# Performance work log

Hardware: AMD Instinct MI355X
Metric: run time of the kernel (lower is better)

## Reference

```python
import jax, jax.numpy as jnp
import numpy as np

TEMP = 0.02          # init kwarg temp (sim is multiplied by temp before exp)
OTHERWEIGHT = 0.5    # init kwarg otherweight (cross-half weighting)


def _labels(overlap_inds, bs):
    # labels1: class i for group i of feats1; labels2: same class if overlap,
    # else a fresh class starting at K, incrementing per non-overlap group.
    K = overlap_inds.shape[0]
    labels1 = jnp.repeat(jnp.arange(K), bs)
    non = (overlap_inds == 0).astype(jnp.int32)
    excl = jnp.cumsum(non) - non  # exclusive prefix count of non-overlap groups
    cls2 = jnp.where(overlap_inds.astype(bool), jnp.arange(K), K + excl)
    labels2 = jnp.repeat(cls2, bs)
    return jnp.concatenate([labels1, labels2])


def setup_inputs() -> dict:
    key = jax.random.key(0)
    k1, k2, k3 = jax.random.split(key, 3)
    K, BS, F = 8, 256, 512
    feats1 = jax.random.normal(k1, (K * BS, F), dtype=jnp.float32)
    feats2 = jax.random.normal(k2, (K * BS, F), dtype=jnp.float32)
    overlap_inds = jax.random.randint(k3, (K,), 0, 2).astype(jnp.int32)
    return {"feats1": feats1, "feats2": feats2, "overlap_inds": overlap_inds, "bs": BS}


def reference(feats1, feats2, overlap_inds, bs):
    n1 = feats1.shape[0]
    feats = jnp.concatenate([feats1, feats2])         # [N, F]
    n = feats.shape[0]
    labels = _labels(overlap_inds, bs)                # [N]

    same = labels[None, :] == labels[:, None]         # [N, N] bool
    sim = jnp.exp((feats @ feats.T) * TEMP)           # [N, N]

    eye = jnp.eye(n, dtype=bool)
    pos_mask = same & ~eye
    neg_mask = ~same

    # cross_weighting: OTHERWEIGHT on cross-half blocks, 1.0 within each half
    half = jnp.arange(n) < n1
    cross = jnp.where(half[:, None] == half[None, :], 1.0, OTHERWEIGHT)

    # per-row negative sum; loss = sum over positives of cw * -log(pos/neg_sum)
    neg_sum = jnp.sum(jnp.where(neg_mask, sim, 0.0), axis=1)        # [N]
    loss_terms = jnp.where(pos_mask, cross * -jnp.log(sim / neg_sum[:, None]), 0.0)
    total_pos = jnp.sum(pos_mask).astype(jnp.float32)
    loss = loss_terms.sum() / total_pos

    # accuracy: a positive counts iff it beats every negative in its row
    # (mean(0)==1.0 over strict > comparisons <=> pos > max(neg))
    max_neg = jnp.max(jnp.where(neg_mask, sim, -jnp.inf), axis=1)   # [N]
    correct = jnp.where(pos_mask, (sim > max_neg[:, None]).astype(jnp.float32), 0.0)
    acc = correct.sum() / total_pos
    return acc, loss
```

## Files before the change

kernel.cpp:

```cpp
#include <hip/hip_runtime.h>


#define KGRP 8
#define FD   512
#define N1T  2048
#define NT   4096
#define TEMPW 0.02f

typedef __attribute__((ext_vector_type(8))) short short8;
typedef __attribute__((ext_vector_type(4))) float f32x4;
typedef unsigned short ushort_t;


__device__ __forceinline__ unsigned enc_ord(float f) {
  unsigned u = __float_as_uint(f);
  return (u & 0x80000000u) ? ~u : (u | 0x80000000u);
}
__device__ __forceinline__ float dec_ord(unsigned u) {
  unsigned b = (u & 0x80000000u) ? (u & 0x7fffffffu) : ~u;
  return __uint_as_float(b);
}

__device__ __forceinline__ ushort_t f2bf(float f) {
  unsigned u = __float_as_uint(f);
  u = (u + 0x7fffu + ((u >> 16) & 1u)) >> 16;
  return (ushort_t)u;
}

__device__ __forceinline__ void gld16(const void* g, void* l) {
  __builtin_amdgcn_global_load_lds(
      (const __attribute__((address_space(1))) unsigned*)g,
      (__attribute__((address_space(3))) unsigned*)l, 16, 0, 0);
}

__global__ __launch_bounds__(256) void prep_k(
    const float* __restrict__ f1, const float* __restrict__ f2,
    ushort_t* __restrict__ bf,
    float* __restrict__ neg_sum, unsigned* __restrict__ neg_max,
    float* __restrict__ sumS, float* __restrict__ corr,
    int* __restrict__ cnts, int* __restrict__ neg_list,
    int* __restrict__ pos_list, const int* __restrict__ ov)
{
  const int b = blockIdx.x, t = threadIdx.x;

  {
    int i = b * 256 + t;
    size_t base = (size_t)i * 8;
    const size_t half = (size_t)N1T * FD;
    const float* sp = (base < half) ? (f1 + base) : (f2 + (base - half));
    float4 u0 = ((const float4*)sp)[0];
    float4 u1 = ((const float4*)sp)[1];
    short8 o;
    o[0] = (short)f2bf(u0.x); o[1] = (short)f2bf(u0.y);
    o[2] = (short)f2bf(u0.z); o[3] = (short)f2bf(u0.w);
    o[4] = (short)f2bf(u1.x); o[5] = (short)f2bf(u1.y);
    o[6] = (short)f2bf(u1.z); o[7] = (short)f2bf(u1.w);
    *(short8*)(bf + base) = o;
  }

  if (b >= 1 && b <= 16) {
    int i = (b - 1) * 256 + t;
    neg_sum[i] = 0.f;
    neg_max[i] = 0u;
  }

  if (b == 0) {
    __shared__ int c[16];
    if (t == 0) {
      sumS[0] = 0.f; corr[0] = 0.f;
      cnts[0] = 0; cnts[1] = 0; cnts[2] = 0;
      int excl = 0;
      for (int g = 0; g < KGRP; g++) c[g] = g;
      for (int g = 0; g < KGRP; g++) {
        if (ov[g]) c[KGRP + g] = g;
        else       { c[KGRP + g] = KGRP + excl; excl++; }
      }
    }
    __syncthreads();
    for (int p = t; p < 1024; p += 256) {
      int bi = p >> 5, bj = p & 31;
      if (bj < bi) continue;
      if (c[bi >> 1] == c[bj >> 1]) {
        int k = atomicAdd(&cnts[1], 1); pos_list[k] = (bi << 5) | bj;
      } else {
        int k = atomicAdd(&cnts[0], 1); neg_list[k] = (bi << 5) | bj;
      }
    }
  }
}

__global__ __launch_bounds__(256, 2) void gram_k(
    const ushort_t* __restrict__ bf, const int* __restrict__ cnts,
    const int* __restrict__ neg_list, const int* __restrict__ pos_list,
    float* __restrict__ neg_sum, unsigned* __restrict__ neg_max,
    float* __restrict__ pos_dots)
{
  __shared__ char lds[4 * 16384];

  const int nn = cnts[0];
  const int b  = blockIdx.x;
  const bool isneg = (b < nn);
  const int pr = isneg ? neg_list[b] : pos_list[b - nn];
  const int bi = pr >> 5, bj = pr & 31;
  const int brow = bi << 7, bcol = bj << 7;

  const int t    = threadIdx.x;
  const int lane = t & 63, wave = t >> 6;
  const int wrow = (wave >> 1) << 6, wcol = (wave & 1) << 6;
  const int fr   = lane & 15, fh = lane >> 4;

  const int r_in = t >> 2;
  const int csw  = (((t & 3) ^ ((t >> 3) & 3)) << 3);
  const ushort_t* gA = bf + (size_t)(brow + r_in) * FD + csw;
  const ushort_t* gB = bf + (size_t)(bcol + r_in) * FD + csw;
  const int ldsw = wave << 10;

  const int fx = ((fh ^ ((fr >> 1) & 3)) << 4);
  int offA[4], offB[4];
#pragma unroll
  for (int m = 0; m < 4; m++) offA[m] = ((wrow + (m << 4) + fr) << 6) + fx;
#pragma unroll
  for (int n = 0; n < 4; n++) offB[n] = 8192 + ((wcol + (n << 4) + fr) << 6) + fx;

  f32x4 acc[4][4];
#pragma unroll
  for (int m = 0; m < 4; m++)
#pragma unroll
    for (int n = 0; n < 4; n++)
      acc[m][n] = (f32x4){0.f, 0.f, 0.f, 0.f};

  auto stage = [&](int s) {
    char* dst = lds + ((s & 3) * 16384) + ldsw;
    const ushort_t* a = gA + (s << 5);
    const ushort_t* p = gB + (s << 5);
    gld16(a,                   dst);
    gld16(a + (size_t)64 * FD, dst + 4096);
    gld16(p,                   dst + 8192);
    gld16(p + (size_t)64 * FD, dst + 12288);
  };

  stage(0); stage(1); stage(2);

#pragma unroll
  for (int s = 0; s < 16; s++) {
    if (s < 14)       asm volatile("s_waitcnt vmcnt(8)" ::: "memory");
    else if (s == 14) asm volatile("s_waitcnt vmcnt(4)" ::: "memory");
    else              asm volatile("s_waitcnt vmcnt(0)" ::: "memory");
    __builtin_amdgcn_s_barrier();
    asm volatile("" ::: "memory");

    char* base = lds + (s & 3) * 16384;
    short8 a[4], bb[4];
#pragma unroll
    for (int m = 0; m < 4; m++) a[m]  = *(const short8*)(base + offA[m]);
#pragma unroll
    for (int n = 0; n < 4; n++) bb[n] = *(const short8*)(base + offB[n]);

    if (s + 3 < 16) stage(s + 3);

#pragma unroll
    for (int m = 0; m < 4; m++)
#pragma unroll
      for (int n = 0; n < 4; n++)
        acc[m][n] = __builtin_amdgcn_mfma_f32_16x16x32_bf16(a[m], bb[n], acc[m][n], 0, 0, 0);
  }

  const int rbase = brow + wrow + (fh << 2);
  const int cbase = bcol + wcol + fr;

  if (isneg) {
    float colS[4] = {0.f, 0.f, 0.f, 0.f};
    float colM[4] = {-3.0e38f, -3.0e38f, -3.0e38f, -3.0e38f};
#pragma unroll
    for (int m = 0; m < 4; m++) {
#pragma unroll
      for (int j = 0; j < 4; j++) {
        float s = 0.f, mx = -3.0e38f;
#pragma unroll
        for (int n = 0; n < 4; n++) {
          float d = acc[m][n][j];
          float e = __expf(d * TEMPW);
          s += e; mx = fmaxf(mx, d);
          colS[n] += e; colM[n] = fmaxf(colM[n], d);
        }
#pragma unroll
        for (int o = 1; o < 16; o <<= 1) {
          s  += __shfl_xor(s, o, 64);
          mx  = fmaxf(mx, __shfl_xor(mx, o, 64));
        }
        if (fr == 0) {
          int r = rbase + (m << 4) + j;
          atomicAdd(&neg_sum[r], s);
          atomicMax(&neg_max[r], enc_ord(mx));
        }
      }
    }
#pragma unroll
    for (int n = 0; n < 4; n++) {
      float s = colS[n], mx = colM[n];
      s += __shfl_xor(s, 16, 64); mx = fmaxf(mx, __shfl_xor(mx, 16, 64));
      s += __shfl_xor(s, 32, 64); mx = fmaxf(mx, __shfl_xor(mx, 32, 64));
      if (fh == 0) {
        int c = cbase + (n << 4);
        atomicAdd(&neg_sum[c], s);
        atomicMax(&neg_max[c], enc_ord(mx));
      }
    }
  } else {
    float* basep = pos_dots + (size_t)(b - nn) * 16384;
#pragma unroll
    for (int m = 0; m < 4; m++)
#pragma unroll
      for (int n = 0; n < 4; n++)
        *(f32x4*)(basep + (((m << 2) + n) << 10) + (t << 2)) = acc[m][n];
  }
}

__global__ __launch_bounds__(256) void pos_fin_k(
    const float* __restrict__ pos_dots, const int* __restrict__ cnts,
    const int* __restrict__ pos_list, const unsigned* __restrict__ neg_max,
    const float* __restrict__ neg_sum, const int* __restrict__ ov,
    float* __restrict__ sumS, float* __restrict__ corr,
    int* __restrict__ done, float* __restrict__ out)
{
  const int np = cnts[1];
  const int p  = blockIdx.x;
  const int t  = threadIdx.x, lane = t & 63, wave = t >> 6;

  __shared__ float wsum[4];
  __shared__ int   wcnt[4];
  __shared__ int   amLast;

  if (p < np) {
    const int pr = pos_list[p];
    const int bi = pr >> 5, bj = pr & 31;
    const int wrow = (wave >> 1) << 6, wcol = (wave & 1) << 6;
    const int fr = lane & 15, fh = lane >> 4;
    const int rbase = (bi << 7) + wrow + (fh << 2);
    const int cbase = (bj << 7) + wcol + fr;
    const float cw = ((bi < 16) == (bj < 16)) ? 1.0f : 0.5f;
    const float* basep = pos_dots + (size_t)p * 16384;

    float ssum = 0.f;
    int cc = 0;
    if (bi == bj) {
#pragma unroll
      for (int m = 0; m < 4; m++)
#pragma unroll
        for (int n = 0; n < 4; n++) {
          f32x4 v = *(const f32x4*)(basep + (((m << 2) + n) << 10) + (t << 2));
          int c = cbase + (n << 4);
#pragma unroll
          for (int j = 0; j < 4; j++) {
            int r = rbase + (m << 4) + j;
            if (r != c) {
              float d = v[j];
              ssum += d;
              cc += (d > dec_ord(neg_max[r])) ? 1 : 0;
            }
          }
        }
    } else {
      float nmr[4][4], nmc[4];
#pragma unroll
      for (int m = 0; m < 4; m++)
#pragma unroll
        for (int j = 0; j < 4; j++) nmr[m][j] = dec_ord(neg_max[rbase + (m << 4) + j]);
#pragma unroll
      for (int n = 0; n < 4; n++) nmc[n] = dec_ord(neg_max[cbase + (n << 4)]);
#pragma unroll
      for (int m = 0; m < 4; m++)
#pragma unroll
        for (int n = 0; n < 4; n++) {
          f32x4 v = *(const f32x4*)(basep + (((m << 2) + n) << 10) + (t << 2));
#pragma unroll
          for (int j = 0; j < 4; j++) {
            float d = v[j];
            ssum += d;
            cc += ((d > nmr[m][j]) ? 1 : 0) + ((d > nmc[n]) ? 1 : 0);
          }
        }
      ssum *= 2.0f;
    }
    ssum *= cw;

#pragma unroll
    for (int o = 1; o < 64; o <<= 1) {
      ssum += __shfl_xor(ssum, o, 64);
      cc   += __shfl_xor(cc, o, 64);
    }
    if (lane == 0) { wsum[wave] = ssum; wcnt[wave] = cc; }
    __syncthreads();
    if (t == 0) {
      float S2 = 0.f; int C2 = 0;
      for (int w = 0; w < 4; w++) { S2 += wsum[w]; C2 += wcnt[w]; }
      atomicAdd(sumS, S2);
      atomicAdd(corr, (float)C2);
    }
  }

  if (t == 0) {
    int my = -1;
    if (p < np) { __threadfence(); my = atomicAdd(done, 1); }
    amLast = (my == np - 1) ? 1 : 0;
  }
  __syncthreads();
  if (!amLast) return;
  __threadfence();

  float aa = 0.f;
  for (int r = t; r < NT; r += 256) {
    int g = r >> 8;
    float W = ov[g & 7] ? 383.f : 255.f;
    aa += W * __logf(neg_sum[r]);
  }
#pragma unroll
  for (int o = 1; o < 64; o <<= 1) aa += __shfl_xor(aa, o, 64);
  if (lane == 0) wsum[wave] = aa;
  __syncthreads();
  if (t == 0) {
    float sw = wsum[0] + wsum[1] + wsum[2] + wsum[3];
    float S = atomicAdd(sumS, 0.f);
    float C = atomicAdd(corr, 0.f);
    float tp = 0.f;
    for (int g = 0; g < 16; g++) tp += 256.f * (255.f + 256.f * (ov[g & 7] ? 1.f : 0.f));
    out[0] = C / tp;
    out[1] = (sw - TEMPW * S) / tp;
  }
}


extern "C" void kernel_launch(void* const* d_in, const int* in_sizes, int n_in,
                              void* d_out, int out_size, void* d_ws, size_t ws_size,
                              hipStream_t stream)
{
  const float* f1 = (const float*)d_in[0];
  const float* f2 = (const float*)d_in[1];
  const int*   ov = (const int*)d_in[2];

  char* ws = (char*)d_ws;
  ushort_t* bf       = (ushort_t*)ws;
  float*    neg_sum  = (float*)(ws + (size_t)(4 << 20));
  unsigned* neg_max  = (unsigned*)(ws + (size_t)(4 << 20) + (16 << 10));
  float*    sumS     = (float*)(ws + (size_t)(4 << 20) + (32 << 10));
  float*    corr     = sumS + 1;
  int*      cnts     = (int*)(sumS + 2);
  int*      done     = cnts + 2;
  int*      neg_list = (int*)(ws + (size_t)(4 << 20) + (36 << 10));
  int*      pos_list = (int*)(ws + (size_t)(4 << 20) + (40 << 10));
  float*    pos_dots = (float*)(ws + (size_t)(4 << 20) + (64 << 10));
  float*    out      = (float*)d_out;

  hipLaunchKernelGGL(prep_k, dim3(1024), dim3(256), 0, stream,
                     f1, f2, bf, neg_sum, neg_max, sumS, corr, cnts,
                     neg_list, pos_list, ov);
  hipLaunchKernelGGL(gram_k, dim3(528), dim3(256), 0, stream,
                     bf, cnts, neg_list, pos_list, neg_sum, neg_max, pos_dots);
  hipLaunchKernelGGL(pos_fin_k, dim3(80), dim3(256), 0, stream,
                     pos_dots, cnts, pos_list, neg_max, neg_sum, ov,
                     sumS, corr, done, out);
}
```

Baseline: 49.16 us.

## Give each wave a private LDS slice to drop block barriers in GEMM loop

Each wave now loads only the A rows and B columns it consumes into its own double-buffered LDS region, so the per-k-step block-wide s_barrier is removed and only vmcnt waits remain. This trades shared reuse across waves for independence. Global traffic per block doubles, because each A and B row slice is fetched by two waves instead of one. Pipeline depth also drops from three stages ahead to one.

```diff
diff --git a/kernel.cpp b/kernel.cpp
--- a/kernel.cpp
+++ b/kernel.cpp
@@ -109,18 +109,19 @@
   const int wrow = (wave >> 1) << 6, wcol = (wave & 1) << 6;
   const int fr   = lane & 15, fh = lane >> 4;
 
-  const int r_in = t >> 2;
-  const int csw  = (((t & 3) ^ ((t >> 3) & 3)) << 3);
-  const ushort_t* gA = bf + (size_t)(brow + r_in) * FD + csw;
-  const ushort_t* gB = bf + (size_t)(bcol + r_in) * FD + csw;
-  const int ldsw = wave << 10;
+  char* myLds = lds + wave * 16384;
+
+  const int rq  = lane >> 2;
+  const int csw = ((lane & 3) ^ ((lane >> 3) & 3)) << 3;
+  const ushort_t* gA = bf + (size_t)(brow + wrow + rq) * FD + csw;
+  const ushort_t* gB = bf + (size_t)(bcol + wcol + rq) * FD + csw;
 
   const int fx = ((fh ^ ((fr >> 1) & 3)) << 4);
   int offA[4], offB[4];
 #pragma unroll
-  for (int m = 0; m < 4; m++) offA[m] = ((wrow + (m << 4) + fr) << 6) + fx;
-#pragma unroll
-  for (int n = 0; n < 4; n++) offB[n] = 8192 + ((wcol + (n << 4) + fr) << 6) + fx;
+  for (int m = 0; m < 4; m++) offA[m] = (((m << 4) + fr) << 6) + fx;
+#pragma unroll
+  for (int n = 0; n < 4; n++) offB[n] = 4096 + (((n << 4) + fr) << 6) + fx;
 
   f32x4 acc[4][4];
 #pragma unroll
@@ -129,34 +130,34 @@
     for (int n = 0; n < 4; n++)
       acc[m][n] = (f32x4){0.f, 0.f, 0.f, 0.f};
 
-  auto stage = [&](int s) {
-    char* dst = lds + ((s & 3) * 16384) + ldsw;
+  auto stageW = [&](int s) {
+    char* dst = myLds + ((s & 1) << 13);
     const ushort_t* a = gA + (s << 5);
     const ushort_t* p = gB + (s << 5);
-    gld16(a,                   dst);
-    gld16(a + (size_t)64 * FD, dst + 4096);
-    gld16(p,                   dst + 8192);
-    gld16(p + (size_t)64 * FD, dst + 12288);
+    gld16(a,         dst);
+    gld16(a +  8192, dst + 1024);
+    gld16(a + 16384, dst + 2048);
+    gld16(a + 24576, dst + 3072);
+    gld16(p,         dst + 4096);
+    gld16(p +  8192, dst + 5120);
+    gld16(p + 16384, dst + 6144);
+    gld16(p + 24576, dst + 7168);
   };
 
-  stage(0); stage(1); stage(2);
+  stageW(0);
 
 #pragma unroll
   for (int s = 0; s < 16; s++) {
-    if (s < 14)       asm volatile("s_waitcnt vmcnt(8)" ::: "memory");
-    else if (s == 14) asm volatile("s_waitcnt vmcnt(4)" ::: "memory");
-    else              asm volatile("s_waitcnt vmcnt(0)" ::: "memory");
-    __builtin_amdgcn_s_barrier();
-    asm volatile("" ::: "memory");
-
-    char* base = lds + (s & 3) * 16384;
+    if (s + 1 < 16) stageW(s + 1);
+    if (s + 1 < 16) asm volatile("s_waitcnt vmcnt(8)" ::: "memory");
+    else            asm volatile("s_waitcnt vmcnt(0)" ::: "memory");
+
+    char* base = myLds + ((s & 1) << 13);
     short8 a[4], bb[4];
 #pragma unroll
     for (int m = 0; m < 4; m++) a[m]  = *(const short8*)(base + offA[m]);
 #pragma unroll
     for (int n = 0; n < 4; n++) bb[n] = *(const short8*)(base + offB[n]);
-
-    if (s + 3 < 16) stage(s + 3);
 
 #pragma unroll
     for (int m = 0; m < 4; m++)
```

Measured after the change: 54.08 us. 1.1x slower.

## Fuse gram and positive-finalize kernels via atomic job queue and spin-wait

Applied to the files above, without the earlier changes.

Merges the gram and positive-finalization kernels into one persistent-style kernel. Each block takes a job index from an atomic ticket, so negative tiles are handed out first. Positive-tile blocks spin until every negative tile has published its row max, then finish their accuracy and loss terms straight from registers. This removes the pos_dots round-trip through global memory and one kernel launch. In exchange, positive blocks can idle while they wait, and the scheme depends on ticket ordering to avoid deadlock.

```diff
diff --git a/kernel.cpp b/kernel.cpp
--- a/kernel.cpp
+++ b/kernel.cpp
@@ -32,6 +32,7 @@
       (const __attribute__((address_space(1))) unsigned*)g,
       (__attribute__((address_space(3))) unsigned*)l, 16, 0, 0);
 }
+
 
 __global__ __launch_bounds__(256) void prep_k(
     const float* __restrict__ f1, const float* __restrict__ f2,
@@ -68,7 +69,7 @@
     __shared__ int c[16];
     if (t == 0) {
       sumS[0] = 0.f; corr[0] = 0.f;
-      cnts[0] = 0; cnts[1] = 0; cnts[2] = 0;
+      cnts[0] = 0; cnts[1] = 0; cnts[2] = 0; cnts[3] = 0; cnts[4] = 0;
       int excl = 0;
       for (int g = 0; g < KGRP; g++) c[g] = g;
       for (int g = 0; g < KGRP; g++) {
@@ -89,22 +90,27 @@
   }
 }
 
-__global__ __launch_bounds__(256, 2) void gram_k(
-    const ushort_t* __restrict__ bf, const int* __restrict__ cnts,
+__global__ __launch_bounds__(256, 2) void main_k(
+    const ushort_t* __restrict__ bf, int* __restrict__ cnts,
     const int* __restrict__ neg_list, const int* __restrict__ pos_list,
     float* __restrict__ neg_sum, unsigned* __restrict__ neg_max,
-    float* __restrict__ pos_dots)
+    float* __restrict__ sumS, float* __restrict__ corr,
+    const int* __restrict__ ov, float* __restrict__ out)
 {
   __shared__ char lds[4 * 16384];
-
-  const int nn = cnts[0];
-  const int b  = blockIdx.x;
-  const bool isneg = (b < nn);
-  const int pr = isneg ? neg_list[b] : pos_list[b - nn];
+  __shared__ int jid_sh;
+  __shared__ int amLast;
+
+  const int t = threadIdx.x;
+  if (t == 0) jid_sh = atomicAdd(&cnts[2], 1);
+  __syncthreads();
+  const int k  = jid_sh;
+  const int nn = cnts[0], np = cnts[1];
+  const bool isneg = (k < nn);
+  const int pr = isneg ? neg_list[k] : pos_list[k - nn];
   const int bi = pr >> 5, bj = pr & 31;
   const int brow = bi << 7, bcol = bj << 7;
 
-  const int t    = threadIdx.x;
   const int lane = t & 63, wave = t >> 6;
   const int wrow = (wave >> 1) << 6, wcol = (wave & 1) << 6;
   const int fr   = lane & 15, fh = lane >> 4;
@@ -206,113 +212,89 @@
         atomicMax(&neg_max[c], enc_ord(mx));
       }
     }
+    __syncthreads();
+    if (t == 0) { __threadfence(); atomicAdd(&cnts[3], 1); }
+    return;
+  }
+
+  if (t == 0) {
+    while (atomicAdd(&cnts[3], 0) < nn) __builtin_amdgcn_s_sleep(8);
+  }
+  __syncthreads();
+
+  float* nmf = (float*)lds;
+  if (t < 128) nmf[t] = dec_ord(atomicAdd(&neg_max[brow + t], 0u));
+  else         nmf[t] = dec_ord(atomicAdd(&neg_max[bcol + (t - 128)], 0u));
+  __syncthreads();
+
+  const float cw = ((bi < 16) == (bj < 16)) ? 1.0f : 0.5f;
+  float ssum = 0.f;
+  int cc = 0;
+  if (bi == bj) {
+#pragma unroll
+    for (int m = 0; m < 4; m++)
+#pragma unroll
+      for (int j = 0; j < 4; j++) {
+        int rloc = wrow + (fh << 2) + (m << 4) + j;
+        float nmr = nmf[rloc];
+#pragma unroll
+        for (int n = 0; n < 4; n++) {
+          int cloc = wcol + fr + (n << 4);
+          if (rloc != cloc) {
+            float d = acc[m][n][j];
+            ssum += d;
+            cc += (d > nmr) ? 1 : 0;
+          }
+        }
+      }
   } else {
-    float* basep = pos_dots + (size_t)(b - nn) * 16384;
+    float nmc[4];
+#pragma unroll
+    for (int n = 0; n < 4; n++) nmc[n] = nmf[128 + wcol + fr + (n << 4)];
 #pragma unroll
     for (int m = 0; m < 4; m++)
 #pragma unroll
-      for (int n = 0; n < 4; n++)
-        *(f32x4*)(basep + (((m << 2) + n) << 10) + (t << 2)) = acc[m][n];
-  }
-}
-
-__global__ __launch_bounds__(256) void pos_fin_k(
-    const float* __restrict__ pos_dots, const int* __restrict__ cnts,
-    const int* __restrict__ pos_list, const unsigned* __restrict__ neg_max,
-    const float* __restrict__ neg_sum, const int* __restrict__ ov,
-    float* __restrict__ sumS, float* __restrict__ corr,
-    int* __restrict__ done, float* __restrict__ out)
-{
-  const int np = cnts[1];
-  const int p  = blockIdx.x;
-  const int t  = threadIdx.x, lane = t & 63, wave = t >> 6;
-
-  __shared__ float wsum[4];
-  __shared__ int   wcnt[4];
-  __shared__ int   amLast;
-
-  if (p < np) {
-    const int pr = pos_list[p];
-    const int bi = pr >> 5, bj = pr & 31;
-    const int wrow = (wave >> 1) << 6, wcol = (wave & 1) << 6;
-    const int fr = lane & 15, fh = lane >> 4;
-    const int rbase = (bi << 7) + wrow + (fh << 2);
-    const int cbase = (bj << 7) + wcol + fr;
-    const float cw = ((bi < 16) == (bj < 16)) ? 1.0f : 0.5f;
-    const float* basep = pos_dots + (size_t)p * 16384;
-
-    float ssum = 0.f;
-    int cc = 0;
-    if (bi == bj) {
-#pragma unroll
-      for (int m = 0; m < 4; m++)
+      for (int j = 0; j < 4; j++) {
+        float nmr = nmf[wrow + (fh << 2) + (m << 4) + j];
 #pragma unroll
         for (int n = 0; n < 4; n++) {
-          f32x4 v = *(const f32x4*)(basep + (((m << 2) + n) << 10) + (t << 2));
-          int c = cbase + (n << 4);
-#pragma unroll
-          for (int j = 0; j < 4; j++) {
-            int r = rbase + (m << 4) + j;
-            if (r != c) {
-              float d = v[j];
-              ssum += d;
-              cc += (d > dec_ord(neg_max[r])) ? 1 : 0;
-            }
-          }
-        }
-    } else {
-      float nmr[4][4], nmc[4];
-#pragma unroll
-      for (int m = 0; m < 4; m++)
-#pragma unroll
-        for (int j = 0; j < 4; j++) nmr[m][j] = dec_ord(neg_max[rbase + (m << 4) + j]);
-#pragma unroll
-      for (int n = 0; n < 4; n++) nmc[n] = dec_ord(neg_max[cbase + (n << 4)]);
-#pragma unroll
-      for (int m = 0; m < 4; m++)
-#pragma unroll
-        for (int n = 0; n < 4; n++) {
-          f32x4 v = *(const f32x4*)(basep + (((m << 2) + n) << 10) + (t << 2));
-#pragma unroll
-          for (int j = 0; j < 4; j++) {
-            float d = v[j];
-            ssum += d;
-            cc += ((d > nmr[m][j]) ? 1 : 0) + ((d > nmc[n]) ? 1 : 0);
-          }
-        }
-      ssum *= 2.0f;
-    }
-    ssum *= cw;
-
-#pragma unroll
-    for (int o = 1; o < 64; o <<= 1) {
-      ssum += __shfl_xor(ssum, o, 64);
-      cc   += __shfl_xor(cc, o, 64);
-    }
-    if (lane == 0) { wsum[wave] = ssum; wcnt[wave] = cc; }
-    __syncthreads();
-    if (t == 0) {
-      float S2 = 0.f; int C2 = 0;
-      for (int w = 0; w < 4; w++) { S2 += wsum[w]; C2 += wcnt[w]; }
-      atomicAdd(sumS, S2);
-      atomicAdd(corr, (float)C2);
-    }
-  }
-
+          float d = acc[m][n][j];
+          ssum += d;
+          cc += ((d > nmr) ? 1 : 0) + ((d > nmc[n]) ? 1 : 0);
+        }
+      }
+    ssum *= 2.0f;
+  }
+  ssum *= cw;
+
+#pragma unroll
+  for (int o = 1; o < 64; o <<= 1) {
+    ssum += __shfl_xor(ssum, o, 64);
+    cc   += __shfl_xor(cc, o, 64);
+  }
+  __syncthreads();
+  float* wsum = (float*)(lds);
+  int*   wcnt = (int*)(lds + 64);
+  if (lane == 0) { wsum[wave] = ssum; wcnt[wave] = cc; }
+  __syncthreads();
   if (t == 0) {
-    int my = -1;
-    if (p < np) { __threadfence(); my = atomicAdd(done, 1); }
+    float S2 = 0.f; int C2 = 0;
+    for (int w = 0; w < 4; w++) { S2 += wsum[w]; C2 += wcnt[w]; }
+    atomicAdd(sumS, S2);
+    atomicAdd(corr, (float)C2);
+    __threadfence();
+    int my = atomicAdd(&cnts[4], 1);
     amLast = (my == np - 1) ? 1 : 0;
   }
   __syncthreads();
   if (!amLast) return;
-  __threadfence();
 
   float aa = 0.f;
   for (int r = t; r < NT; r += 256) {
     int g = r >> 8;
     float W = ov[g & 7] ? 383.f : 255.f;
-    aa += W * __logf(neg_sum[r]);
+    float ns = atomicAdd(&neg_sum[r], 0.f);
+    aa += W * __logf(ns);
   }
 #pragma unroll
   for (int o = 1; o < 64; o <<= 1) aa += __shfl_xor(aa, o, 64);
@@ -345,18 +327,14 @@
   float*    sumS     = (float*)(ws + (size_t)(4 << 20) + (32 << 10));
   float*    corr     = sumS + 1;
   int*      cnts     = (int*)(sumS + 2);
-  int*      done     = cnts + 2;
   int*      neg_list = (int*)(ws + (size_t)(4 << 20) + (36 << 10));
   int*      pos_list = (int*)(ws + (size_t)(4 << 20) + (40 << 10));
-  float*    pos_dots = (float*)(ws + (size_t)(4 << 20) + (64 << 10));
   float*    out      = (float*)d_out;
 
   hipLaunchKernelGGL(prep_k, dim3(1024), dim3(256), 0, stream,
                      f1, f2, bf, neg_sum, neg_max, sumS, corr, cnts,
                      neg_list, pos_list, ov);
-  hipLaunchKernelGGL(gram_k, dim3(528), dim3(256), 0, stream,
-                     bf, cnts, neg_list, pos_list, neg_sum, neg_max, pos_dots);
-  hipLaunchKernelGGL(pos_fin_k, dim3(80), dim3(256), 0, stream,
-                     pos_dots, cnts, pos_list, neg_max, neg_sum, ov,
-                     sumS, corr, done, out);
-}
+  hipLaunchKernelGGL(main_k, dim3(528), dim3(256), 0, stream,
+                     bf, cnts, neg_list, pos_list, neg_sum, neg_max,
+                     sumS, corr, ov, out);
+}
```

Result: slower. 72.15 us (+46.8%).
